# Kernel tuning notes

Measured on AMD Instinct MI355X. Metric: run time of the kernel, lower is better.

## Reference

```python
import jax, jax.numpy as jnp
import numpy as np

N_HEAD, D_HEAD, D_MODEL, MAX_LEN = 16, 64, 1024, 64
T, B = 1024, 4
SCALE = 1.0 / D_HEAD ** 0.5


def setup_inputs() -> dict:
    key = jax.random.key(0)
    k1, k2, k3, k4 = jax.random.split(key, 4)
    s = 0.02
    w = jax.random.normal(k1, (T, B, D_MODEL), jnp.float32)
    Wqkv = jax.random.normal(k2, (3 * N_HEAD * D_HEAD, D_MODEL), jnp.float32) * s
    pos_emb = jax.random.normal(k3, (2 * MAX_LEN + 1, D_HEAD), jnp.float32) * s
    Wo = jax.random.normal(k4, (D_MODEL, N_HEAD * D_HEAD), jnp.float32) * s
    i = jnp.arange(T)
    # causal mask, 3D path of the original: [qlen, klen, bsz], True = masked
    attn_mask = jnp.broadcast_to((i[None, :] > i[:, None])[:, :, None], (T, T, B))
    return {"w": w, "attn_mask": attn_mask, "Wqkv": Wqkv, "pos_emb": pos_emb, "Wo": Wo}


def reference(w, attn_mask, Wqkv, pos_emb, Wo):
    qlen, bsz, _ = w.shape
    klen = qlen
    # qkv projection (no bias), chunk into q, k, v
    heads = jnp.einsum('tbd,ed->tbe', w, Wqkv)            # [T, B, 3*H*Dh]
    q, k, v = jnp.split(heads, 3, axis=-1)
    q = q.reshape(qlen, bsz, N_HEAD, D_HEAD).transpose(1, 2, 0, 3) * SCALE  # [B,H,T,Dh]
    k = k.reshape(klen, bsz, N_HEAD, D_HEAD).transpose(1, 2, 0, 3)
    v = v.reshape(klen, bsz, N_HEAD, D_HEAD).transpose(1, 2, 0, 3)
    # learnable relative position embeddings r[q_pos, k_pos, Dh]
    i = jnp.arange(klen)
    rel = jnp.clip(i[None, :] - i[:, None], -MAX_LEN, MAX_LEN) + MAX_LEN   # [T, T]
    r = pos_emb[rel]                                                       # [T, T, Dh]
    # content score + relative-position score (q already scaled)
    qk = jnp.einsum('bhqd,bhkd->bhqk', q, k)
    qr = jnp.einsum('bhqd,qkd->bhqk', q, r)
    score = qk + qr                                                        # [B,H,T,T]
    m = attn_mask.transpose(2, 0, 1)[:, None]                              # [B,1,T,T]
    score = jnp.where(m, -jnp.inf, score)
    attn = jax.nn.softmax(score, axis=-1)                                  # coverage
    # content context + position context
    ctx = jnp.einsum('bhqk,bhkd->bhqd', attn, v) + jnp.einsum('bhqk,qkd->bhqd', attn, r)
    attn_vec = ctx.transpose(0, 2, 1, 3).reshape(bsz, qlen, N_HEAD * D_HEAD)
    out = jnp.einsum('bte,de->btd', attn_vec, Wo)                          # [B,T,D]
    return jnp.swapaxes(out, 0, 1)                                         # [T,B,D]
```

## Files before the change

### kernel.cpp

```cpp
#include <hip/hip_runtime.h>
#include <hip/hip_bf16.h>
#include <math.h>

#define N_HEAD 16
#define D_HEAD 64
#define T_SEQ 1024
#define BATCH 4
#define QSCALE 0.180336879f

typedef float f32x4 __attribute__((ext_vector_type(4)));
typedef short bf16x8 __attribute__((ext_vector_type(8)));
typedef short bf16x4v __attribute__((ext_vector_type(4)));

#define AS1(p) ((const __attribute__((address_space(1))) void*)(p))
#define AS3(p) ((__attribute__((address_space(3))) void*)(p))

__device__ inline bf16x8 ld8(const __hip_bfloat16* p) {
    bf16x4v lo = *(const bf16x4v*)p;
    bf16x4v hi = *(const bf16x4v*)(p + 4);
    return __builtin_shufflevector(lo, hi, 0, 1, 2, 3, 4, 5, 6, 7);
}

__global__ __launch_bounds__(256) void cast_all(
    const float* __restrict__ s0, __hip_bfloat16* __restrict__ d0, int n0,
    const float* __restrict__ s1, __hip_bfloat16* __restrict__ d1, int n1,
    const float* __restrict__ s2, __hip_bfloat16* __restrict__ d2, int n2) {
    int i = (blockIdx.x * 256 + threadIdx.x) * 8;
    const float* src;
    __hip_bfloat16* dst;
    if (i < n0) { src = s0 + i; dst = d0 + i; }
    else if ((i -= n0) < n1) { src = s1 + i; dst = d1 + i; }
    else if ((i -= n1) < n2) { src = s2 + i; dst = d2 + i; }
    else return;
    float4 a = *(const float4*)src;
    float4 b = *(const float4*)(src + 4);
    __hip_bfloat16 t[8];
    t[0] = __float2bfloat16(a.x); t[1] = __float2bfloat16(a.y);
    t[2] = __float2bfloat16(a.z); t[3] = __float2bfloat16(a.w);
    t[4] = __float2bfloat16(b.x); t[5] = __float2bfloat16(b.y);
    t[6] = __float2bfloat16(b.z); t[7] = __float2bfloat16(b.w);
    *(uint4*)dst = *(const uint4*)t;
}

__global__ __launch_bounds__(256) void qkv_gemm_mfma(
    const __hip_bfloat16* __restrict__ A,
    const __hip_bfloat16* __restrict__ B,
    const float* __restrict__ P,
    __hip_bfloat16* __restrict__ Qb, __hip_bfloat16* __restrict__ Kb,
    __hip_bfloat16* __restrict__ Vtb) {
    constexpr int Kd = 1024;
    __shared__ __hip_bfloat16 As[128 * 32];
    __shared__ __hip_bfloat16 Bs[128 * 32];
    const int tid = threadIdx.x;
    const int w = tid >> 6, lane = tid & 63;
    const int lanelo = lane & 15, quad = lane >> 4;
    const int wm = (w >> 1) * 64, wn = (w & 1) * 64;

    const int bid = blockIdx.x;
    const int xcd = bid & 7, r = bid >> 3;
    const int ly = r / 12, lx = r % 12;
    const int by = (xcd >> 1) * 8 + ly;
    const int bx = (xcd & 1) * 12 + lx;
    const int m0 = by * 128, n0 = bx * 128;

    const __hip_bfloat16* Ag = A + (size_t)(m0 + w * 16 + (lane >> 2)) * Kd + (lane & 3) * 8;
    const __hip_bfloat16* Bg = B + (size_t)(n0 + w * 16 + (lane >> 2)) * Kd + (lane & 3) * 8;
    __hip_bfloat16* AsW0 = As + w * 16 * 32;
    __hip_bfloat16* AsW1 = As + (64 + w * 16) * 32;
    __hip_bfloat16* BsW0 = Bs + w * 16 * 32;
    __hip_bfloat16* BsW1 = Bs + (64 + w * 16) * 32;

    f32x4 acc[4][4];
#pragma unroll
    for (int i = 0; i < 4; i++)
#pragma unroll
        for (int j = 0; j < 4; j++) acc[i][j] = (f32x4){0.f, 0.f, 0.f, 0.f};

    for (int k0 = 0; k0 < Kd; k0 += 32) {
        __syncthreads();
        __builtin_amdgcn_global_load_lds(AS1(Ag + k0), AS3(AsW0), 16, 0, 0);
        __builtin_amdgcn_global_load_lds(AS1(Ag + 64 * Kd + k0), AS3(AsW1), 16, 0, 0);
        __builtin_amdgcn_global_load_lds(AS1(Bg + k0), AS3(BsW0), 16, 0, 0);
        __builtin_amdgcn_global_load_lds(AS1(Bg + 64 * Kd + k0), AS3(BsW1), 16, 0, 0);
        __syncthreads();
        bf16x8 af[4], bfr[4];
#pragma unroll
        for (int i = 0; i < 4; i++)
            af[i] = *(const bf16x8*)(As + (wm + i * 16 + lanelo) * 32 + quad * 8);
#pragma unroll
        for (int j = 0; j < 4; j++)
            bfr[j] = *(const bf16x8*)(Bs + (wn + j * 16 + lanelo) * 32 + quad * 8);
#pragma unroll
        for (int i = 0; i < 4; i++)
#pragma unroll
            for (int j = 0; j < 4; j++)
                acc[i][j] = __builtin_amdgcn_mfma_f32_16x16x32_bf16(af[i], bfr[j], acc[i][j], 0, 0, 0);
    }

    const int part = n0 >> 10;
    float p0v[4] = {0.f, 0.f, 0.f, 0.f};
    if (part == 2) {
#pragma unroll
        for (int j = 0; j < 4; j++) p0v[j] = P[j * 16 + lanelo];
    }
#pragma unroll
    for (int i = 0; i < 4; i++)
#pragma unroll
        for (int j = 0; j < 4; j++)
#pragma unroll
            for (int reg = 0; reg < 4; reg++) {
                const int row = m0 + wm + i * 16 + quad * 4 + reg;
                const int col = n0 + wn + j * 16 + lanelo;
                const int t = row >> 2, b = row & 3;
                const int e = col & 1023, h = e >> 6, d = e & 63;
                const float v = acc[i][j][reg];
                if (part == 0)
                    Qb[((size_t)(b * 16 + h) * 1024 + t) * 64 + d] = __float2bfloat16(v * QSCALE);
                else if (part == 1)
                    Kb[((size_t)(b * 16 + h) * 1024 + t) * 64 + d] = __float2bfloat16(v);
                else
                    Vtb[((size_t)(b * 16 + h) * 64 + d) * 1024 + t] = __float2bfloat16(v + p0v[j]);
            }
}

__global__ __launch_bounds__(256) void out_gemm_mfma(
    const __hip_bfloat16* __restrict__ A,
    const __hip_bfloat16* __restrict__ B,
    float* __restrict__ out) {
    constexpr int Kd = 1024;
    __shared__ __hip_bfloat16 As[128 * 64];
    __shared__ __hip_bfloat16 Bs[64 * 64];
    const int tid = threadIdx.x;
    const int w = tid >> 6, lane = tid & 63;
    const int lanelo = lane & 15, quad = lane >> 4;
    const int wm = (w >> 1) * 64, wn = (w & 1) * 32;
    const int m0 = blockIdx.y * 128, n0 = blockIdx.x * 64;

    const int sr = lane >> 3;
    const int sc = ((lane & 7) ^ sr) * 8;
    const __hip_bfloat16* Ag = A + (size_t)(m0 + w * 32 + sr) * Kd + sc;
    const __hip_bfloat16* Bg = B + (size_t)(n0 + w * 16 + sr) * Kd + sc;
    __hip_bfloat16* AsW = As + w * 2048;
    __hip_bfloat16* BsW = Bs + w * 1024;

    f32x4 acc[4][2];
#pragma unroll
    for (int i = 0; i < 4; i++)
#pragma unroll
        for (int j = 0; j < 2; j++) acc[i][j] = (f32x4){0.f, 0.f, 0.f, 0.f};

    const int cswz = lanelo & 7;

    for (int k0 = 0; k0 < Kd; k0 += 64) {
        __syncthreads();
#pragma unroll
        for (int i = 0; i < 4; i++)
            __builtin_amdgcn_global_load_lds(AS1(Ag + k0 + i * 8 * Kd), AS3(AsW + i * 512), 16, 0, 0);
#pragma unroll
        for (int i = 0; i < 2; i++)
            __builtin_amdgcn_global_load_lds(AS1(Bg + k0 + i * 8 * Kd), AS3(BsW + i * 512), 16, 0, 0);
        __syncthreads();
#pragma unroll
        for (int h = 0; h < 2; h++) {
            const int c16 = (((h * 4 + quad) ^ cswz)) * 8;
            bf16x8 af[4], bfr[2];
#pragma unroll
            for (int i = 0; i < 4; i++)
                af[i] = *(const bf16x8*)(As + (size_t)(wm + i * 16 + lanelo) * 64 + c16);
#pragma unroll
            for (int j = 0; j < 2; j++)
                bfr[j] = *(const bf16x8*)(Bs + (size_t)(wn + j * 16 + lanelo) * 64 + c16);
#pragma unroll
            for (int i = 0; i < 4; i++)
#pragma unroll
                for (int j = 0; j < 2; j++)
                    acc[i][j] = __builtin_amdgcn_mfma_f32_16x16x32_bf16(af[i], bfr[j], acc[i][j], 0, 0, 0);
        }
    }

#pragma unroll
    for (int i = 0; i < 4; i++)
#pragma unroll
        for (int j = 0; j < 2; j++)
#pragma unroll
            for (int reg = 0; reg < 4; reg++) {
                const int row = m0 + wm + i * 16 + quad * 4 + reg;
                const int col = n0 + wn + j * 16 + lanelo;
                const int b = row >> 10, t = row & 1023;
                out[(size_t)(t * 4 + b) * 1024 + col] = acc[i][j][reg];
            }
}

__global__ __launch_bounds__(256) void flash_attn(
    const __hip_bfloat16* __restrict__ Qb,
    const __hip_bfloat16* __restrict__ Kb,
    const __hip_bfloat16* __restrict__ Vtb,
    const float* __restrict__ P,
    __hip_bfloat16* __restrict__ av) {
    __shared__ __hip_bfloat16 Ks[64][72];
    __shared__ __hip_bfloat16 Vs[64][72];
    __shared__ __hip_bfloat16 Pl[4][16][68];
    __shared__ __hip_bfloat16 Pband[4][2][16][68];
    __shared__ __hip_bfloat16 QPl[4][2][16][66];

    const int px = blockIdx.x;
    const int TB = 15 - px, TS = px;
    const int bh = blockIdx.y;
    const int b = bh >> 4, h = bh & 15;
    const int tid = threadIdx.x;
    const int w = tid >> 6, lane = tid & 63;
    const int lanelo = lane & 15, quad = lane >> 4;
    const size_t qkbase = (size_t)bh * 1024 * 64;
    const size_t vbase  = (size_t)bh * 64 * 1024;

    const int sr = tid >> 2;
    const int sc = (tid & 3) << 4;
    const __hip_bfloat16* kgb = Kb + qkbase + (size_t)sr * 64 + sc;
    const __hip_bfloat16* vgb = Vtb + vbase + (size_t)sr * 1024 + sc;

    {
        short* pb = (short*)&Pband[w][0][0][0];
        for (int i = lane; i < 2 * 16 * 68; i += 64) pb[i] = 0;
    }

    bf16x8 aqb0, aqb1, aqs0, aqs1;
    {
        const __hip_bfloat16* qrb = Qb + qkbase + (size_t)(TB * 64 + w * 16 + lanelo) * 64;
        aqb0 = *(const bf16x8*)(qrb + quad * 8);
        aqb1 = *(const bf16x8*)(qrb + 32 + quad * 8);
        const __hip_bfloat16* qrs = Qb + qkbase + (size_t)(TS * 64 + w * 16 + lanelo) * 64;
        aqs0 = *(const bf16x8*)(qrs + quad * 8);
        aqs1 = *(const bf16x8*)(qrs + 32 + quad * 8);
    }

#pragma unroll
    for (int jj = 0; jj < 5; jj++) {
        const float* prow = P + (size_t)(jj * 16 + lanelo) * 64 + quad * 8;
        float4 pa = *(const float4*)prow;
        float4 pb = *(const float4*)(prow + 4);
        float4 pc = *(const float4*)(prow + 32);
        float4 pd = *(const float4*)(prow + 36);
        __hip_bfloat16 t0[8], t1[8];
        t0[0] = __float2bfloat16(pa.x); t0[1] = __float2bfloat16(pa.y);
        t0[2] = __float2bfloat16(pa.z); t0[3] = __float2bfloat16(pa.w);
        t0[4] = __float2bfloat16(pb.x); t0[5] = __float2bfloat16(pb.y);
        t0[6] = __float2bfloat16(pb.z); t0[7] = __float2bfloat16(pb.w);
        t1[0] = __float2bfloat16(pc.x); t1[1] = __float2bfloat16(pc.y);
        t1[2] = __float2bfloat16(pc.z); t1[3] = __float2bfloat16(pc.w);
        t1[4] = __float2bfloat16(pd.x); t1[5] = __float2bfloat16(pd.y);
        t1[6] = __float2bfloat16(pd.z); t1[7] = __float2bfloat16(pd.w);
        f32x4 accB = (f32x4){0.f, 0.f, 0.f, 0.f};
        accB = __builtin_amdgcn_mfma_f32_16x16x32_bf16(aqb0, *(const bf16x8*)t0, accB, 0, 0, 0);
        accB = __builtin_amdgcn_mfma_f32_16x16x32_bf16(aqb1, *(const bf16x8*)t1, accB, 0, 0, 0);
        f32x4 accS = (f32x4){0.f, 0.f, 0.f, 0.f};
        accS = __builtin_amdgcn_mfma_f32_16x16x32_bf16(aqs0, *(const bf16x8*)t0, accS, 0, 0, 0);
        accS = __builtin_amdgcn_mfma_f32_16x16x32_bf16(aqs1, *(const bf16x8*)t1, accS, 0, 0, 0);
#pragma unroll
        for (int reg = 0; reg < 4; reg++) {
            QPl[w][0][quad * 4 + reg][jj * 16 + lanelo] = __float2bfloat16(accB[reg]);
            QPl[w][1][quad * 4 + reg][jj * 16 + lanelo] = __float2bfloat16(accS[reg]);
        }
    }
    float qp0b[4], qp0s[4];
#pragma unroll
    for (int reg = 0; reg < 4; reg++) {
        qp0b[reg] = (float)QPl[w][0][quad * 4 + reg][0];
        qp0s[reg] = (float)QPl[w][1][quad * 4 + reg][0];
    }

    f32x4 o_accB[4], o_lB, o_accS[4], o_lS;
#pragma unroll
    for (int dt = 0; dt < 4; dt++) {
        o_accB[dt] = (f32x4){0.f, 0.f, 0.f, 0.f};
        o_accS[dt] = (f32x4){0.f, 0.f, 0.f, 0.f};
    }
    o_lB = (f32x4){0.f, 0.f, 0.f, 0.f};
    o_lS = (f32x4){0.f, 0.f, 0.f, 0.f};
    const short one_bf = 0x3F80;
    const bf16x8 vones = {one_bf, one_bf, one_bf, one_bf, one_bf, one_bf, one_bf, one_bf};

    auto do_qtile = [&](int tq, int Tq, const bf16x8& a0, const bf16x8& a1,
                        const float* qp0, f32x4* o_acc, f32x4& o_l, int kt) {
        f32x4 s_acc[4];
#pragma unroll
        for (int ct = 0; ct < 4; ct++) {
            bf16x8 b0 = *(const bf16x8*)&Ks[ct * 16 + lanelo][quad * 8];
            bf16x8 b1 = *(const bf16x8*)&Ks[ct * 16 + lanelo][32 + quad * 8];
            f32x4 acc = (f32x4){0.f, 0.f, 0.f, 0.f};
            acc = __builtin_amdgcn_mfma_f32_16x16x32_bf16(a0, b0, acc, 0, 0, 0);
            acc = __builtin_amdgcn_mfma_f32_16x16x32_bf16(a1, b1, acc, 0, 0, 0);
            s_acc[ct] = acc;
        }
        const int q0 = Tq * 64 + w * 16;
        const int obase = q0 - kt * 64;
        if (kt < Tq - 1) {
#pragma unroll
            for (int ct = 0; ct < 4; ct++)
#pragma unroll
                for (int reg = 0; reg < 4; reg++) {
                    const float p = __builtin_exp2f(s_acc[ct][reg] + qp0[reg]);
                    Pl[w][quad * 4 + reg][ct * 16 + lanelo] = __float2bfloat16(p);
                }
        } else {
#pragma unroll
            for (int ct = 0; ct < 4; ct++)
#pragma unroll
                for (int reg = 0; reg < 4; reg++) {
                    const int rloc = quad * 4 + reg;
                    const int kl = ct * 16 + lanelo;
                    const int o = obase + rloc - kl;
                    const int idx = (o >= 64 || o < 0) ? 0 : (64 - o);
                    const float add = (float)QPl[w][tq][rloc][idx];
                    const float p = (o < 0) ? 0.f : __builtin_exp2f(s_acc[ct][reg] + add);
                    const __hip_bfloat16 pbv = __float2bfloat16(p);
                    Pl[w][rloc][kl] = pbv;
                    if (o >= 0 && o <= 63) Pband[w][tq][rloc][63 - o] = pbv;
                }
        }
#pragma unroll
        for (int c = 0; c < 2; c++) {
            bf16x8 ap = ld8(&Pl[w][lanelo][c * 32 + quad * 8]);
#pragma unroll
            for (int dt = 0; dt < 4; dt++) {
                bf16x8 bv = *(const bf16x8*)&Vs[dt * 16 + lanelo][c * 32 + quad * 8];
                o_acc[dt] = __builtin_amdgcn_mfma_f32_16x16x32_bf16(ap, bv, o_acc[dt], 0, 0, 0);
            }
            o_l = __builtin_amdgcn_mfma_f32_16x16x32_bf16(ap, vones, o_l, 0, 0, 0);
        }
    };

    uint4 rk0, rk1, rv0, rv1;
    rk0 = *(const uint4*)(kgb);
    rk1 = *(const uint4*)(kgb + 8);
    rv0 = *(const uint4*)(vgb);
    rv1 = *(const uint4*)(vgb + 8);

    for (int kt = 0; kt <= TB; kt++) {
        __syncthreads();
        *(uint4*)&Ks[sr][sc]     = rk0;
        *(uint4*)&Ks[sr][sc + 8] = rk1;
        *(uint4*)&Vs[sr][sc]     = rv0;
        *(uint4*)&Vs[sr][sc + 8] = rv1;
        if (kt < TB) {
            const __hip_bfloat16* kg = kgb + (size_t)(kt + 1) * 4096;
            const __hip_bfloat16* vg = vgb + (size_t)(kt + 1) * 64;
            rk0 = *(const uint4*)(kg);
            rk1 = *(const uint4*)(kg + 8);
            rv0 = *(const uint4*)(vg);
            rv1 = *(const uint4*)(vg + 8);
        }
        __syncthreads();

        do_qtile(0, TB, aqb0, aqb1, qp0b, o_accB, o_lB, kt);
        if (kt <= TS) do_qtile(1, TS, aqs0, aqs1, qp0s, o_accS, o_lS, kt);
    }

#pragma unroll
    for (int tq = 0; tq < 2; tq++) {
        f32x4* o_acc = tq == 0 ? o_accB : o_accS;
        f32x4& o_l   = tq == 0 ? o_lB : o_lS;
        const int q0 = (tq == 0 ? TB : TS) * 64 + w * 16;
#pragma unroll
        for (int c = 0; c < 2; c++) {
            bf16x8 ab = ld8(&Pband[w][tq][lanelo][c * 32 + quad * 8]);
#pragma unroll
            for (int dt = 0; dt < 4; dt++) {
                const int d = dt * 16 + lanelo;
                const float p0 = P[d];
                __hip_bfloat16 tb[8];
#pragma unroll
                for (int jj = 0; jj < 8; jj++) {
                    const int kk = c * 32 + quad * 8 + jj;
                    tb[jj] = __float2bfloat16(P[(kk + 1) * 64 + d] - p0);
                }
                o_acc[dt] = __builtin_amdgcn_mfma_f32_16x16x32_bf16(ab, *(const bf16x8*)tb, o_acc[dt], 0, 0, 0);
            }
        }
        float rinv[4];
#pragma unroll
        for (int reg = 0; reg < 4; reg++) rinv[reg] = 1.0f / o_l[reg];
#pragma unroll
        for (int dt = 0; dt < 4; dt++) {
            const int cdim = dt * 16 + lanelo;
#pragma unroll
            for (int reg = 0; reg < 4; reg++) {
                const int q = q0 + quad * 4 + reg;
                av[((size_t)(b * 1024 + q)) * 1024 + h * 64 + cdim] =
                    __float2bfloat16(o_acc[dt][reg] * rinv[reg]);
            }
        }
    }
}

extern "C" void kernel_launch(void* const* d_in, const int* in_sizes, int n_in,
                              void* d_out, int out_size, void* d_ws, size_t ws_size,
                              hipStream_t stream) {
    const float* w       = (const float*)d_in[0];
    const float* Wqkv    = (const float*)d_in[2];
    const float* pos_emb = (const float*)d_in[3];
    const float* Wo      = (const float*)d_in[4];
    float* out = (float*)d_out;

    const size_t SZ = (size_t)BATCH * N_HEAD * T_SEQ * D_HEAD;
    __hip_bfloat16* wb     = (__hip_bfloat16*)d_ws;
    __hip_bfloat16* Wqkvb  = wb + SZ;
    __hip_bfloat16* Wob    = Wqkvb + 3 * 1024 * 1024;
    __hip_bfloat16* Qb     = Wob + 1024 * 1024;
    __hip_bfloat16* Kb     = Qb + SZ;
    __hip_bfloat16* Vtb    = Kb + SZ;
    __hip_bfloat16* AVb    = Vtb + SZ;

    const int n_w = 4096 * 1024, n_wqkv = 3072 * 1024, n_wo = 1024 * 1024;
    const int n_tot = n_w + n_wqkv + n_wo;
    cast_all<<<n_tot / 2048, 256, 0, stream>>>(w, wb, n_w, Wqkv, Wqkvb, n_wqkv, Wo, Wob, n_wo);

    qkv_gemm_mfma<<<dim3(768), 256, 0, stream>>>(wb, Wqkvb, pos_emb, Qb, Kb, Vtb);
    flash_attn<<<dim3(8, 64), 256, 0, stream>>>(Qb, Kb, Vtb, pos_emb, AVb);
    out_gemm_mfma<<<dim3(1024 / 64, 4096 / 128), 256, 0, stream>>>(AVb, Wob, out);
}
```

Baseline: 190.1 us.

## Fuse Wo cast into attention, add MFMA priority hints, drop XCD tile remap

The Wo fp32-to-bf16 conversion moves out of the cast kernel and into the flash attention prologue, where each of the 512 blocks converts one chunk, which shortens the cast kernel. s_setprio hints are wrapped around the MFMA sections of the attention inner loop to favour matrix issue over the exp and softmax code. The QKV GEMM drops its XCD-aware block swizzle and goes back to a plain 2D grid, which may hurt L2 locality.

After: 187.1 us. Within noise of the previous version (-1.6%).

```diff
diff --git a/kernel.cpp b/kernel.cpp
--- a/kernel.cpp
+++ b/kernel.cpp
@@ -23,14 +23,12 @@
 
 __global__ __launch_bounds__(256) void cast_all(
     const float* __restrict__ s0, __hip_bfloat16* __restrict__ d0, int n0,
-    const float* __restrict__ s1, __hip_bfloat16* __restrict__ d1, int n1,
-    const float* __restrict__ s2, __hip_bfloat16* __restrict__ d2, int n2) {
+    const float* __restrict__ s1, __hip_bfloat16* __restrict__ d1, int n1) {
     int i = (blockIdx.x * 256 + threadIdx.x) * 8;
     const float* src;
     __hip_bfloat16* dst;
     if (i < n0) { src = s0 + i; dst = d0 + i; }
     else if ((i -= n0) < n1) { src = s1 + i; dst = d1 + i; }
-    else if ((i -= n1) < n2) { src = s2 + i; dst = d2 + i; }
     else return;
     float4 a = *(const float4*)src;
     float4 b = *(const float4*)(src + 4);
@@ -55,13 +53,7 @@
     const int w = tid >> 6, lane = tid & 63;
     const int lanelo = lane & 15, quad = lane >> 4;
     const int wm = (w >> 1) * 64, wn = (w & 1) * 64;
-
-    const int bid = blockIdx.x;
-    const int xcd = bid & 7, r = bid >> 3;
-    const int ly = r / 12, lx = r % 12;
-    const int by = (xcd >> 1) * 8 + ly;
-    const int bx = (xcd & 1) * 12 + lx;
-    const int m0 = by * 128, n0 = bx * 128;
+    const int m0 = blockIdx.y * 128, n0 = blockIdx.x * 128;
 
     const __hip_bfloat16* Ag = A + (size_t)(m0 + w * 16 + (lane >> 2)) * Kd + (lane & 3) * 8;
     const __hip_bfloat16* Bg = B + (size_t)(n0 + w * 16 + (lane >> 2)) * Kd + (lane & 3) * 8;
@@ -196,6 +188,8 @@
     const __hip_bfloat16* __restrict__ Kb,
     const __hip_bfloat16* __restrict__ Vtb,
     const float* __restrict__ P,
+    const float* __restrict__ Wo,
+    __hip_bfloat16* __restrict__ Wob,
     __hip_bfloat16* __restrict__ av) {
     __shared__ __hip_bfloat16 Ks[64][72];
     __shared__ __hip_bfloat16 Vs[64][72];
@@ -208,6 +202,19 @@
     const int bh = blockIdx.y;
     const int b = bh >> 4, h = bh & 15;
     const int tid = threadIdx.x;
+
+    {
+        const int gid = (bh * 8 + px) * 256 + tid;
+        const float4 a = *(const float4*)(Wo + (size_t)gid * 8);
+        const float4 c = *(const float4*)(Wo + (size_t)gid * 8 + 4);
+        __hip_bfloat16 t[8];
+        t[0] = __float2bfloat16(a.x); t[1] = __float2bfloat16(a.y);
+        t[2] = __float2bfloat16(a.z); t[3] = __float2bfloat16(a.w);
+        t[4] = __float2bfloat16(c.x); t[5] = __float2bfloat16(c.y);
+        t[6] = __float2bfloat16(c.z); t[7] = __float2bfloat16(c.w);
+        *(uint4*)(Wob + (size_t)gid * 8) = *(const uint4*)t;
+    }
+
     const int w = tid >> 6, lane = tid & 63;
     const int lanelo = lane & 15, quad = lane >> 4;
     const size_t qkbase = (size_t)bh * 1024 * 64;
@@ -282,6 +289,7 @@
     auto do_qtile = [&](int tq, int Tq, const bf16x8& a0, const bf16x8& a1,
                         const float* qp0, f32x4* o_acc, f32x4& o_l, int kt) {
         f32x4 s_acc[4];
+        __builtin_amdgcn_s_setprio(1);
 #pragma unroll
         for (int ct = 0; ct < 4; ct++) {
             bf16x8 b0 = *(const bf16x8*)&Ks[ct * 16 + lanelo][quad * 8];
@@ -291,6 +299,7 @@
             acc = __builtin_amdgcn_mfma_f32_16x16x32_bf16(a1, b1, acc, 0, 0, 0);
             s_acc[ct] = acc;
         }
+        __builtin_amdgcn_s_setprio(0);
         const int q0 = Tq * 64 + w * 16;
         const int obase = q0 - kt * 64;
         if (kt < Tq - 1) {
@@ -317,6 +326,7 @@
                     if (o >= 0 && o <= 63) Pband[w][tq][rloc][63 - o] = pbv;
                 }
         }
+        __builtin_amdgcn_s_setprio(1);
 #pragma unroll
         for (int c = 0; c < 2; c++) {
             bf16x8 ap = ld8(&Pl[w][lanelo][c * 32 + quad * 8]);
@@ -327,6 +337,7 @@
             }
             o_l = __builtin_amdgcn_mfma_f32_16x16x32_bf16(ap, vones, o_l, 0, 0, 0);
         }
+        __builtin_amdgcn_s_setprio(0);
     };
 
     uint4 rk0, rk1, rv0, rv1;
@@ -410,11 +421,11 @@
     __hip_bfloat16* Vtb    = Kb + SZ;
     __hip_bfloat16* AVb    = Vtb + SZ;
 
-    const int n_w = 4096 * 1024, n_wqkv = 3072 * 1024, n_wo = 1024 * 1024;
-    const int n_tot = n_w + n_wqkv + n_wo;
-    cast_all<<<n_tot / 2048, 256, 0, stream>>>(w, wb, n_w, Wqkv, Wqkvb, n_wqkv, Wo, Wob, n_wo);
-
-    qkv_gemm_mfma<<<dim3(768), 256, 0, stream>>>(wb, Wqkvb, pos_emb, Qb, Kb, Vtb);
-    flash_attn<<<dim3(8, 64), 256, 0, stream>>>(Qb, Kb, Vtb, pos_emb, AVb);
+    const int n_w = 4096 * 1024, n_wqkv = 3072 * 1024;
+    const int n_tot = n_w + n_wqkv;
+    cast_all<<<n_tot / 2048, 256, 0, stream>>>(w, wb, n_w, Wqkv, Wqkvb, n_wqkv);
+
+    qkv_gemm_mfma<<<dim3(3072 / 128, 4096 / 128), 256, 0, stream>>>(wb, Wqkvb, pos_emb, Qb, Kb, Vtb);
+    flash_attn<<<dim3(8, 64), 256, 0, stream>>>(Qb, Kb, Vtb, pos_emb, Wo, Wob, AVb);
     out_gemm_mfma<<<dim3(1024 / 64, 4096 / 128), 256, 0, stream>>>(AVb, Wob, out);
 }
```
